# Kernel tuning notes

Hardware: AMD Instinct MI355X
Metric: run time of the kernel (lower is better)

## Reference

```python
import jax, jax.numpy as jnp
import numpy as np

NUM_QUBITS = 4
NUM_LAYERS = 3


def _ry(state, theta, wire):
    # state: (N,2,2,2,2) real amplitudes; RY(theta) on `wire` (angle scalar or (N,))
    st = jnp.moveaxis(state, wire + 1, -1)
    c = jnp.cos(theta * 0.5)
    s = jnp.sin(theta * 0.5)
    if jnp.ndim(c) == 1:  # per-sample angle -> broadcast over remaining qubit axes
        shape = (c.shape[0],) + (1,) * (st.ndim - 2)
        c = c.reshape(shape)
        s = s.reshape(shape)
    s0, s1 = st[..., 0], st[..., 1]
    new = jnp.stack([c * s0 - s * s1, s * s0 + c * s1], axis=-1)
    return jnp.moveaxis(new, -1, wire + 1)


def _cnot(state, control, target):
    st = jnp.moveaxis(state, (control + 1, target + 1), (-2, -1))
    new = jnp.stack([st[..., 0, :], st[..., 1, ::-1]], axis=-2)
    return jnp.moveaxis(new, (-2, -1), (control + 1, target + 1))


def _circuit(angles, params):
    # angles: (N,4) input rotations; params: (L,4,1) shared variational angles
    N = angles.shape[0]
    state = jnp.zeros((N, 2, 2, 2, 2), angles.dtype).at[:, 0, 0, 0, 0].set(1.0)
    for q in range(NUM_QUBITS):
        state = _ry(state, angles[:, q], q)
    for l in range(NUM_LAYERS):
        for q in range(NUM_QUBITS):
            state = _ry(state, params[l, q, 0], q)
        for q in range(NUM_QUBITS - 1):
            state = _cnot(state, q, q + 1)
    probs = state * state  # amplitudes are real (only RY/CNOT)
    meas = []
    for w in range(NUM_QUBITS):
        axes = tuple(a for a in range(1, NUM_QUBITS + 1) if a != w + 1)
        p = probs.sum(axes)  # (N,2)
        meas.append(p[:, 0] - p[:, 1])  # <Z_w>
    return jnp.stack(meas, axis=-1)  # (N,4)


def setup_inputs() -> dict:
    key = jax.random.key(0)
    k1, k2, k3, k4, k5 = jax.random.split(key, 5)
    B = 8192
    return {
        "x": jax.random.uniform(k1, (B, 1, 28, 28), dtype=jnp.float32),
        "params": jax.random.normal(k2, (NUM_LAYERS, NUM_QUBITS, 1), dtype=jnp.float32),
        "res_w": jax.random.normal(k3, (4, 1, 1, 1), dtype=jnp.float32),
        "cls_w": jax.random.normal(k4, (10, 784), dtype=jnp.float32) * 0.03,
        "cls_b": jax.random.normal(k5, (10,), dtype=jnp.float32) * 0.03,
    }


def reference(x, params, res_w, cls_w, cls_b):
    B = x.shape[0]
    img = x.reshape(B, 28, 28)
    # extract 2x2 patches, element order (r,c),(r,c+1),(r+1,c),(r+1,c+1)
    patches = img.reshape(B, 14, 2, 14, 2).transpose(0, 1, 3, 2, 4).reshape(B, 196, 4)
    # per-patch-index min/max over batch and the 4 elements (matches patch.min()/max())
    mn = patches.min(axis=(0, 2), keepdims=True)
    mx = patches.max(axis=(0, 2), keepdims=True)
    ang = (patches - mn) / (mx - mn + 1e-8) * jnp.pi
    meas = _circuit(ang.reshape(B * 196, 4), params)  # (B*196, 4)
    out = meas.reshape(B, 196 * 4).reshape(B, 4, 14, 14)  # matches torch.cat(...).view
    # res_conv: 1x1 conv, stride 2, no bias -> strided pixel scaled per out-channel
    res = img[:, ::2, ::2][:, None, :, :] * res_w.reshape(1, 4, 1, 1)
    out = out + res
    logits = out.reshape(B, -1) @ cls_w.T + cls_b
    return jax.nn.log_softmax(logits, axis=-1)
```

## Files before the change

kernel.cpp:

```cpp
#include <hip/hip_runtime.h>
#include <math.h>

#define NP 196
#define PI_F 3.14159265358979323846f

__device__ __forceinline__ unsigned fkey(float f) {
  unsigned u = __float_as_uint(f);
  return u ^ ((unsigned)((int)u >> 31) | 0x80000000u);
}
__device__ __forceinline__ float funkey(unsigned k) {
  unsigned u = (k & 0x80000000u) ? (k ^ 0x80000000u) : ~k;
  return __uint_as_float(u);
}

__global__ void __launch_bounds__(256) precompute_kernel(
    const float* __restrict__ params, const float* __restrict__ res_w,
    const float* __restrict__ cls_w, float* __restrict__ U,
    float* __restrict__ W2, unsigned* __restrict__ mn,
    unsigned* __restrict__ mx) {
  const int tid = threadIdx.x;
  if (blockIdx.x == 0) {
    if (tid < NP) { mn[tid] = 0xFFFFFFFFu; mx[tid] = 0u; }
    if (tid < 16) {
      float cp[12], sp[12];
#pragma unroll
      for (int l = 0; l < 12; ++l) __sincosf(0.5f * params[l], &sp[l], &cp[l]);
      float st[16];
#pragma unroll
      for (int i = 0; i < 16; ++i) st[i] = 0.f;
      st[tid] = 1.f;
#pragma unroll
      for (int l = 0; l < 3; ++l) {
#pragma unroll
        for (int q = 0; q < 4; ++q) {
          const float cq = cp[l * 4 + q], sq = sp[l * 4 + q];
          const int m = 8 >> q;
#pragma unroll
          for (int idx = 0; idx < 16; ++idx) {
            if (idx & m) continue;
            float v0 = st[idx], v1 = st[idx | m];
            st[idx] = cq * v0 - sq * v1;
            st[idx | m] = sq * v0 + cq * v1;
          }
        }
#pragma unroll
        for (int q = 0; q < 3; ++q) {
          const int mc = 8 >> q, mt = 4 >> q;
#pragma unroll
          for (int idx = 0; idx < 16; ++idx) {
            if ((idx & mc) && !(idx & mt)) {
              float t0 = st[idx];
              st[idx] = st[idx | mt];
              st[idx | mt] = t0;
            }
          }
        }
      }
#pragma unroll
      for (int i = 0; i < 16; ++i) U[i * 16 + tid] = st[i];
    }
  }
  for (int t = blockIdx.x * 256 + tid; t < 10 * NP; t += 8 * 256) {
    int k = t / NP, p = t - k * NP;
    float s = 0.f;
#pragma unroll
    for (int c = 0; c < 4; ++c) s += res_w[c] * cls_w[k * 784 + c * NP + p];
    W2[t] = s;
  }
}

__global__ void __launch_bounds__(256) minmax_kernel(
    const float* __restrict__ x, unsigned* __restrict__ mn,
    unsigned* __restrict__ mx, int imgs, int B) {
  __shared__ float pmn[392], pmx[392];
  const int t = threadIdx.x;
  const int img0 = blockIdx.x * imgs;
  if (t < NP) {
    const float* base = x + (size_t)img0 * 784 + 4 * t;
    float mn0 = 3.4e38f, mx0 = -3.4e38f, mn1 = 3.4e38f, mx1 = -3.4e38f;
    const int nimg = (img0 + imgs <= B) ? imgs : (B - img0);
#pragma unroll 4
    for (int m = 0; m < nimg; ++m) {
      float4 v = *(const float4*)(base + (size_t)m * 784);
      mn0 = fminf(mn0, fminf(v.x, v.y));
      mx0 = fmaxf(mx0, fmaxf(v.x, v.y));
      mn1 = fminf(mn1, fminf(v.z, v.w));
      mx1 = fmaxf(mx1, fmaxf(v.z, v.w));
    }
    const int r = (4 * t) / 28;
    const int jj = ((4 * t) - 28 * r) >> 1;
    pmn[r * 14 + jj] = mn0;
    pmx[r * 14 + jj] = mx0;
    pmn[r * 14 + jj + 1] = mn1;
    pmx[r * 14 + jj + 1] = mx1;
  }
  __syncthreads();
  if (t < NP) {
    const int i = t / 14, j = t - i * 14;
    const int f0 = (2 * i) * 14 + j, f1 = f0 + 14;
    atomicMin(&mn[t], fkey(fminf(pmn[f0], pmn[f1])));
    atomicMax(&mx[t], fkey(fmaxf(pmx[f0], pmx[f1])));
  }
}

__global__ void __launch_bounds__(256, 6) circuit_kernel(
    const float* __restrict__ x, const unsigned* __restrict__ mnk,
    const unsigned* __restrict__ mxk, const float* __restrict__ Ug,
    float4* __restrict__ gmeas, int G) {
  __shared__ float sU[256];
  __shared__ float smn[NP], ssc[NP];
  const int tid = threadIdx.x;
  sU[tid] = Ug[tid];
  if (tid < NP) {
    const float mnv = funkey(mnk[tid]);
    const float mxv = funkey(mxk[tid]);
    smn[tid] = mnv;
    ssc[tid] = (0.5f * PI_F) / (mxv - mnv + 1e-8f);
  }
  __syncthreads();

  const int g = blockIdx.x * 256 + tid;
  if (g >= G) return;
  const int b = g / NP;
  const int p = g - b * NP;
  const int i = p / 14, j = p - i * 14;

  const float* px = x + (size_t)b * 784 + (2 * i) * 28 + 2 * j;
  const float2 r0 = *(const float2*)px;
  const float2 r1 = *(const float2*)(px + 28);
  const float mnv = smn[p], sc = ssc[p];

  float cc[4], ss[4];
  __sincosf((r0.x - mnv) * sc, &ss[0], &cc[0]);
  __sincosf((r0.y - mnv) * sc, &ss[1], &cc[1]);
  __sincosf((r1.x - mnv) * sc, &ss[2], &cc[2]);
  __sincosf((r1.y - mnv) * sc, &ss[3], &cc[3]);

  float st[16];
  {
    const float A[4] = {cc[0] * cc[1], cc[0] * ss[1], ss[0] * cc[1], ss[0] * ss[1]};
    const float Bq[4] = {cc[2] * cc[3], cc[2] * ss[3], ss[2] * cc[3], ss[2] * ss[3]};
#pragma unroll
    for (int idx = 0; idx < 16; ++idx) st[idx] = A[idx >> 2] * Bq[idx & 3];
  }

  float z0 = 0.f, z1 = 0.f, z2 = 0.f, z3 = 0.f;
#pragma unroll
  for (int i2 = 0; i2 < 16; ++i2) {
    const float4 u0 = *(const float4*)&sU[i2 * 16 + 0];
    const float4 u1 = *(const float4*)&sU[i2 * 16 + 4];
    const float4 u2 = *(const float4*)&sU[i2 * 16 + 8];
    const float4 u3 = *(const float4*)&sU[i2 * 16 + 12];
    float f = u0.x * st[0];
    f = fmaf(u0.y, st[1], f);
    f = fmaf(u0.z, st[2], f);
    f = fmaf(u0.w, st[3], f);
    f = fmaf(u1.x, st[4], f);
    f = fmaf(u1.y, st[5], f);
    f = fmaf(u1.z, st[6], f);
    f = fmaf(u1.w, st[7], f);
    f = fmaf(u2.x, st[8], f);
    f = fmaf(u2.y, st[9], f);
    f = fmaf(u2.z, st[10], f);
    f = fmaf(u2.w, st[11], f);
    f = fmaf(u3.x, st[12], f);
    f = fmaf(u3.y, st[13], f);
    f = fmaf(u3.z, st[14], f);
    f = fmaf(u3.w, st[15], f);
    if (!(i2 & 8)) z0 = fmaf(f, f, z0);
    if (!(i2 & 4)) z1 = fmaf(f, f, z1);
    if (!(i2 & 2)) z2 = fmaf(f, f, z2);
    if (!(i2 & 1)) z3 = fmaf(f, f, z3);
  }
  gmeas[g] = make_float4(fmaf(2.f, z0, -1.f), fmaf(2.f, z1, -1.f),
                         fmaf(2.f, z2, -1.f), fmaf(2.f, z3, -1.f));
}

__global__ void __launch_bounds__(256) cls_kernel(
    const float4* __restrict__ gmeas, const float* __restrict__ x,
    const float* __restrict__ W2, const float4* __restrict__ cls_w4,
    const float* __restrict__ cls_b, float* __restrict__ out, int B) {
  const int wv = (blockIdx.x * 256 + threadIdx.x) >> 6;
  const int lane = threadIdx.x & 63;
  if (wv >= B) return;
  const float4* mrow = gmeas + (size_t)wv * NP;
  const float* xrow = x + (size_t)wv * 784;

  float acc[10];
#pragma unroll
  for (int k = 0; k < 10; ++k) acc[k] = 0.f;

  for (int t4 = lane; t4 < NP; t4 += 64) {
    const float4 v = mrow[t4];
#pragma unroll
    for (int k = 0; k < 10; ++k) {
      const float4 w = cls_w4[k * NP + t4];
      acc[k] = fmaf(v.x, w.x, fmaf(v.y, w.y, fmaf(v.z, w.z, fmaf(v.w, w.w, acc[k]))));
    }
  }
  for (int p = lane; p < NP; p += 64) {
    const int i = p / 14, j = p - i * 14;
    const float v = xrow[(2 * i) * 28 + 2 * j];
#pragma unroll
    for (int k = 0; k < 10; ++k) acc[k] = fmaf(v, W2[k * NP + p], acc[k]);
  }
#pragma unroll
  for (int k = 0; k < 10; ++k) {
    float a = acc[k];
#pragma unroll
    for (int off = 32; off > 0; off >>= 1) a += __shfl_down(a, off, 64);
    acc[k] = a;
  }
  if (lane == 0) {
    float lg[10];
#pragma unroll
    for (int k = 0; k < 10; ++k) lg[k] = acc[k] + cls_b[k];
    float m = lg[0];
#pragma unroll
    for (int k = 1; k < 10; ++k) m = fmaxf(m, lg[k]);
    float s = 0.f;
#pragma unroll
    for (int k = 0; k < 10; ++k) s += __expf(lg[k] - m);
    const float lse = m + __logf(s);
#pragma unroll
    for (int k = 0; k < 10; ++k) out[(size_t)wv * 10 + k] = lg[k] - lse;
  }
}

extern "C" void kernel_launch(void* const* d_in, const int* in_sizes, int n_in,
                              void* d_out, int out_size, void* d_ws, size_t ws_size,
                              hipStream_t stream) {
  const float* x      = (const float*)d_in[0];
  const float* params = (const float*)d_in[1];
  const float* res_w  = (const float*)d_in[2];
  const float* cls_w  = (const float*)d_in[3];
  const float* cls_b  = (const float*)d_in[4];
  float* out = (float*)d_out;
  const int B = in_sizes[0] / 784;

  unsigned* mn = (unsigned*)d_ws;
  unsigned* mx = mn + NP;
  float* U  = (float*)(mx + NP);
  float* W2 = U + 256;
  float* gmeas = W2 + 10 * NP;

  precompute_kernel<<<8, 256, 0, stream>>>(params, res_w, cls_w, U, W2, mn, mx);

  const int imgs = 16;
  const int nblk1 = (B + imgs - 1) / imgs;
  minmax_kernel<<<nblk1, 256, 0, stream>>>(x, mn, mx, imgs, B);

  const int G = B * NP;
  circuit_kernel<<<(G + 255) / 256, 256, 0, stream>>>(x, mn, mx, U, (float4*)gmeas, G);

  cls_kernel<<<(B * 64 + 255) / 256, 256, 0, stream>>>((const float4*)gmeas, x, W2,
                                                       (const float4*)cls_w, cls_b, out, B);
}
```

Measured before the change: 131.2 us.

## Fuse all stages into one cooperative persistent kernel with grid syncs

Replaces the four launches (precompute, minmax, circuit, classifier) with a single cooperative kernel of 512 persistent blocks that use grid.sync between phases. The min/max reduction now writes per-block partials and reduces them in a second phase instead of using global atomics. The circuit phase processes two samples per thread for more instruction-level parallelism, with split FMA chains. This removes launch gaps and atomic contention, but adds grid-wide barriers and a fixed grid size that may under-occupy the GPU.

```diff
diff --git a/kernel.cpp b/kernel.cpp
--- a/kernel.cpp
+++ b/kernel.cpp
@@ -1,8 +1,12 @@
 #include <hip/hip_runtime.h>
+#include <hip/hip_cooperative_groups.h>
 #include <math.h>
+
+namespace cg = cooperative_groups;
 
 #define NP 196
 #define PI_F 3.14159265358979323846f
+#define GRID 512
 
 __device__ __forceinline__ unsigned fkey(float f) {
   unsigned u = __float_as_uint(f);
@@ -13,73 +17,104 @@
   return __uint_as_float(u);
 }
 
-__global__ void __launch_bounds__(256) precompute_kernel(
-    const float* __restrict__ params, const float* __restrict__ res_w,
-    const float* __restrict__ cls_w, float* __restrict__ U,
-    float* __restrict__ W2, unsigned* __restrict__ mn,
-    unsigned* __restrict__ mx) {
+struct Samp {
+  float st[16];
+  const float* px;
+};
+
+__device__ __forceinline__ void load_state(const float* __restrict__ x,
+                                           const float* __restrict__ smn,
+                                           const float* __restrict__ ssc,
+                                           int g, float st[16]) {
+  const int b = g / NP;
+  const int p = g - b * NP;
+  const int i = p / 14, j = p - i * 14;
+  const float* px = x + (size_t)b * 784 + (2 * i) * 28 + 2 * j;
+  const float2 r0 = *(const float2*)px;
+  const float2 r1 = *(const float2*)(px + 28);
+  const float mnv = smn[p], sc = ssc[p];
+  float cc[4], ss[4];
+  __sincosf((r0.x - mnv) * sc, &ss[0], &cc[0]);
+  __sincosf((r0.y - mnv) * sc, &ss[1], &cc[1]);
+  __sincosf((r1.x - mnv) * sc, &ss[2], &cc[2]);
+  __sincosf((r1.y - mnv) * sc, &ss[3], &cc[3]);
+  const float A[4] = {cc[0] * cc[1], cc[0] * ss[1], ss[0] * cc[1], ss[0] * ss[1]};
+  const float Bq[4] = {cc[2] * cc[3], cc[2] * ss[3], ss[2] * cc[3], ss[2] * ss[3]};
+#pragma unroll
+  for (int idx = 0; idx < 16; ++idx) st[idx] = A[idx >> 2] * Bq[idx & 3];
+}
+
+__global__ void __launch_bounds__(256, 4) fused_kernel(
+    const float* __restrict__ x, const float* __restrict__ params,
+    const float* __restrict__ res_w, const float* __restrict__ cls_w,
+    const float* __restrict__ cls_b, float* __restrict__ out,
+    float* __restrict__ Ug, float* __restrict__ W2,
+    float* __restrict__ mnf, float* __restrict__ scf,
+    unsigned* __restrict__ pmn_g, unsigned* __restrict__ pmx_g,
+    float4* __restrict__ gmeas, int B, int ipb) {
+  cg::grid_group grid = cg::this_grid();
   const int tid = threadIdx.x;
-  if (blockIdx.x == 0) {
-    if (tid < NP) { mn[tid] = 0xFFFFFFFFu; mx[tid] = 0u; }
-    if (tid < 16) {
-      float cp[12], sp[12];
-#pragma unroll
-      for (int l = 0; l < 12; ++l) __sincosf(0.5f * params[l], &sp[l], &cp[l]);
-      float st[16];
-#pragma unroll
-      for (int i = 0; i < 16; ++i) st[i] = 0.f;
-      st[tid] = 1.f;
-#pragma unroll
-      for (int l = 0; l < 3; ++l) {
-#pragma unroll
-        for (int q = 0; q < 4; ++q) {
-          const float cq = cp[l * 4 + q], sq = sp[l * 4 + q];
-          const int m = 8 >> q;
-#pragma unroll
-          for (int idx = 0; idx < 16; ++idx) {
-            if (idx & m) continue;
-            float v0 = st[idx], v1 = st[idx | m];
-            st[idx] = cq * v0 - sq * v1;
-            st[idx | m] = sq * v0 + cq * v1;
-          }
+  const int blk = blockIdx.x;
+  const int lane = tid & 63;
+  const int wave = tid >> 6;
+
+  __shared__ float pmn[392], pmx[392];
+  __shared__ float sU[256];
+  __shared__ float smn[NP], ssc[NP];
+  __shared__ unsigned rmn[4], rmx[4];
+
+  if (blk == 0 && tid < 16) {
+    float cp[12], sp[12];
+#pragma unroll
+    for (int l = 0; l < 12; ++l) __sincosf(0.5f * params[l], &sp[l], &cp[l]);
+    float st[16];
+#pragma unroll
+    for (int i = 0; i < 16; ++i) st[i] = 0.f;
+    st[tid] = 1.f;
+#pragma unroll
+    for (int l = 0; l < 3; ++l) {
+#pragma unroll
+      for (int q = 0; q < 4; ++q) {
+        const float cq = cp[l * 4 + q], sq = sp[l * 4 + q];
+        const int m = 8 >> q;
+#pragma unroll
+        for (int idx = 0; idx < 16; ++idx) {
+          if (idx & m) continue;
+          float v0 = st[idx], v1 = st[idx | m];
+          st[idx] = cq * v0 - sq * v1;
+          st[idx | m] = sq * v0 + cq * v1;
         }
-#pragma unroll
-        for (int q = 0; q < 3; ++q) {
-          const int mc = 8 >> q, mt = 4 >> q;
-#pragma unroll
-          for (int idx = 0; idx < 16; ++idx) {
-            if ((idx & mc) && !(idx & mt)) {
-              float t0 = st[idx];
-              st[idx] = st[idx | mt];
-              st[idx | mt] = t0;
-            }
+      }
+#pragma unroll
+      for (int q = 0; q < 3; ++q) {
+        const int mc = 8 >> q, mt = 4 >> q;
+#pragma unroll
+        for (int idx = 0; idx < 16; ++idx) {
+          if ((idx & mc) && !(idx & mt)) {
+            float t0 = st[idx];
+            st[idx] = st[idx | mt];
+            st[idx | mt] = t0;
           }
         }
       }
-#pragma unroll
-      for (int i = 0; i < 16; ++i) U[i * 16 + tid] = st[i];
-    }
-  }
-  for (int t = blockIdx.x * 256 + tid; t < 10 * NP; t += 8 * 256) {
+    }
+#pragma unroll
+    for (int i = 0; i < 16; ++i) Ug[i * 16 + tid] = st[i];
+  }
+
+  for (int t = blk * 256 + tid; t < 10 * NP; t += GRID * 256) {
     int k = t / NP, p = t - k * NP;
     float s = 0.f;
 #pragma unroll
     for (int c = 0; c < 4; ++c) s += res_w[c] * cls_w[k * 784 + c * NP + p];
     W2[t] = s;
   }
-}
-
-__global__ void __launch_bounds__(256) minmax_kernel(
-    const float* __restrict__ x, unsigned* __restrict__ mn,
-    unsigned* __restrict__ mx, int imgs, int B) {
-  __shared__ float pmn[392], pmx[392];
-  const int t = threadIdx.x;
-  const int img0 = blockIdx.x * imgs;
-  if (t < NP) {
-    const float* base = x + (size_t)img0 * 784 + 4 * t;
+
+  if (tid < NP) {
+    const int img0 = blk * ipb;
+    const int nimg = min(ipb, B - img0);
+    const float* base = x + (size_t)img0 * 784 + 4 * tid;
     float mn0 = 3.4e38f, mx0 = -3.4e38f, mn1 = 3.4e38f, mx1 = -3.4e38f;
-    const int nimg = (img0 + imgs <= B) ? imgs : (B - img0);
-#pragma unroll 4
     for (int m = 0; m < nimg; ++m) {
       float4 v = *(const float4*)(base + (size_t)m * 784);
       mn0 = fminf(mn0, fminf(v.x, v.y));
@@ -87,143 +122,161 @@
       mn1 = fminf(mn1, fminf(v.z, v.w));
       mx1 = fmaxf(mx1, fmaxf(v.z, v.w));
     }
-    const int r = (4 * t) / 28;
-    const int jj = ((4 * t) - 28 * r) >> 1;
+    const int r = (4 * tid) / 28;
+    const int jj = ((4 * tid) - 28 * r) >> 1;
     pmn[r * 14 + jj] = mn0;
     pmx[r * 14 + jj] = mx0;
     pmn[r * 14 + jj + 1] = mn1;
     pmx[r * 14 + jj + 1] = mx1;
   }
   __syncthreads();
-  if (t < NP) {
-    const int i = t / 14, j = t - i * 14;
+  if (tid < NP) {
+    const int i = tid / 14, j = tid - i * 14;
     const int f0 = (2 * i) * 14 + j, f1 = f0 + 14;
-    atomicMin(&mn[t], fkey(fminf(pmn[f0], pmn[f1])));
-    atomicMax(&mx[t], fkey(fmaxf(pmx[f0], pmx[f1])));
-  }
-}
-
-__global__ void __launch_bounds__(256, 6) circuit_kernel(
-    const float* __restrict__ x, const unsigned* __restrict__ mnk,
-    const unsigned* __restrict__ mxk, const float* __restrict__ Ug,
-    float4* __restrict__ gmeas, int G) {
-  __shared__ float sU[256];
-  __shared__ float smn[NP], ssc[NP];
-  const int tid = threadIdx.x;
+    pmn_g[blk * NP + tid] = fkey(fminf(pmn[f0], pmn[f1]));
+    pmx_g[blk * NP + tid] = fkey(fmaxf(pmx[f0], pmx[f1]));
+  }
+
+  grid.sync();
+
+  if (blk < NP) {
+    unsigned kmn = 0xFFFFFFFFu, kmx = 0u;
+    for (int w = tid; w < GRID; w += 256) {
+      kmn = min(kmn, pmn_g[w * NP + blk]);
+      kmx = max(kmx, pmx_g[w * NP + blk]);
+    }
+#pragma unroll
+    for (int off = 32; off > 0; off >>= 1) {
+      kmn = min(kmn, (unsigned)__shfl_down(kmn, off, 64));
+      kmx = max(kmx, (unsigned)__shfl_down(kmx, off, 64));
+    }
+    if (lane == 0) { rmn[wave] = kmn; rmx[wave] = kmx; }
+    __syncthreads();
+    if (tid == 0) {
+      unsigned fmn = min(min(rmn[0], rmn[1]), min(rmn[2], rmn[3]));
+      unsigned fmx = max(max(rmx[0], rmx[1]), max(rmx[2], rmx[3]));
+      const float mnv = funkey(fmn), mxv = funkey(fmx);
+      mnf[blk] = mnv;
+      scf[blk] = (0.5f * PI_F) / (mxv - mnv + 1e-8f);
+    }
+  }
+
+  grid.sync();
+
   sU[tid] = Ug[tid];
-  if (tid < NP) {
-    const float mnv = funkey(mnk[tid]);
-    const float mxv = funkey(mxk[tid]);
-    smn[tid] = mnv;
-    ssc[tid] = (0.5f * PI_F) / (mxv - mnv + 1e-8f);
-  }
+  if (tid < NP) { smn[tid] = mnf[tid]; ssc[tid] = scf[tid]; }
   __syncthreads();
 
-  const int g = blockIdx.x * 256 + tid;
-  if (g >= G) return;
-  const int b = g / NP;
-  const int p = g - b * NP;
-  const int i = p / 14, j = p - i * 14;
-
-  const float* px = x + (size_t)b * 784 + (2 * i) * 28 + 2 * j;
-  const float2 r0 = *(const float2*)px;
-  const float2 r1 = *(const float2*)(px + 28);
-  const float mnv = smn[p], sc = ssc[p];
-
-  float cc[4], ss[4];
-  __sincosf((r0.x - mnv) * sc, &ss[0], &cc[0]);
-  __sincosf((r0.y - mnv) * sc, &ss[1], &cc[1]);
-  __sincosf((r1.x - mnv) * sc, &ss[2], &cc[2]);
-  __sincosf((r1.y - mnv) * sc, &ss[3], &cc[3]);
-
-  float st[16];
-  {
-    const float A[4] = {cc[0] * cc[1], cc[0] * ss[1], ss[0] * cc[1], ss[0] * ss[1]};
-    const float Bq[4] = {cc[2] * cc[3], cc[2] * ss[3], ss[2] * cc[3], ss[2] * ss[3]};
-#pragma unroll
-    for (int idx = 0; idx < 16; ++idx) st[idx] = A[idx >> 2] * Bq[idx & 3];
-  }
-
-  float z0 = 0.f, z1 = 0.f, z2 = 0.f, z3 = 0.f;
-#pragma unroll
-  for (int i2 = 0; i2 < 16; ++i2) {
-    const float4 u0 = *(const float4*)&sU[i2 * 16 + 0];
-    const float4 u1 = *(const float4*)&sU[i2 * 16 + 4];
-    const float4 u2 = *(const float4*)&sU[i2 * 16 + 8];
-    const float4 u3 = *(const float4*)&sU[i2 * 16 + 12];
-    float f = u0.x * st[0];
-    f = fmaf(u0.y, st[1], f);
-    f = fmaf(u0.z, st[2], f);
-    f = fmaf(u0.w, st[3], f);
-    f = fmaf(u1.x, st[4], f);
-    f = fmaf(u1.y, st[5], f);
-    f = fmaf(u1.z, st[6], f);
-    f = fmaf(u1.w, st[7], f);
-    f = fmaf(u2.x, st[8], f);
-    f = fmaf(u2.y, st[9], f);
-    f = fmaf(u2.z, st[10], f);
-    f = fmaf(u2.w, st[11], f);
-    f = fmaf(u3.x, st[12], f);
-    f = fmaf(u3.y, st[13], f);
-    f = fmaf(u3.z, st[14], f);
-    f = fmaf(u3.w, st[15], f);
-    if (!(i2 & 8)) z0 = fmaf(f, f, z0);
-    if (!(i2 & 4)) z1 = fmaf(f, f, z1);
-    if (!(i2 & 2)) z2 = fmaf(f, f, z2);
-    if (!(i2 & 1)) z3 = fmaf(f, f, z3);
-  }
-  gmeas[g] = make_float4(fmaf(2.f, z0, -1.f), fmaf(2.f, z1, -1.f),
-                         fmaf(2.f, z2, -1.f), fmaf(2.f, z3, -1.f));
-}
-
-__global__ void __launch_bounds__(256) cls_kernel(
-    const float4* __restrict__ gmeas, const float* __restrict__ x,
-    const float* __restrict__ W2, const float4* __restrict__ cls_w4,
-    const float* __restrict__ cls_b, float* __restrict__ out, int B) {
-  const int wv = (blockIdx.x * 256 + threadIdx.x) >> 6;
-  const int lane = threadIdx.x & 63;
-  if (wv >= B) return;
-  const float4* mrow = gmeas + (size_t)wv * NP;
-  const float* xrow = x + (size_t)wv * 784;
-
-  float acc[10];
-#pragma unroll
-  for (int k = 0; k < 10; ++k) acc[k] = 0.f;
-
-  for (int t4 = lane; t4 < NP; t4 += 64) {
-    const float4 v = mrow[t4];
+  const int G = B * NP;
+  const int nGB = (G + 255) / 256;
+  for (int gb = blk; gb < nGB; gb += 2 * GRID) {
+    const int g0 = gb * 256 + tid;
+    const int gb1 = gb + GRID;
+    const bool has1 = gb1 < nGB;
+    const int g1 = (has1 ? gb1 : gb) * 256 + tid;
+
+    float st0[16], st1[16];
+    load_state(x, smn, ssc, g0, st0);
+    load_state(x, smn, ssc, g1, st1);
+
+    float z0a = 0.f, z1a = 0.f, z2a = 0.f, z3a = 0.f;
+    float z0b = 0.f, z1b = 0.f, z2b = 0.f, z3b = 0.f;
+#pragma unroll
+    for (int i2 = 0; i2 < 16; ++i2) {
+      const float4 u0 = *(const float4*)&sU[i2 * 16 + 0];
+      const float4 u1 = *(const float4*)&sU[i2 * 16 + 4];
+      const float4 u2 = *(const float4*)&sU[i2 * 16 + 8];
+      const float4 u3 = *(const float4*)&sU[i2 * 16 + 12];
+      float fa = u0.x * st0[0];
+      fa = fmaf(u0.y, st0[1], fa);
+      fa = fmaf(u0.z, st0[2], fa);
+      fa = fmaf(u0.w, st0[3], fa);
+      float fb = u1.x * st0[4];
+      fb = fmaf(u1.y, st0[5], fb);
+      fb = fmaf(u1.z, st0[6], fb);
+      fb = fmaf(u1.w, st0[7], fb);
+      float fc = u2.x * st0[8];
+      fc = fmaf(u2.y, st0[9], fc);
+      fc = fmaf(u2.z, st0[10], fc);
+      fc = fmaf(u2.w, st0[11], fc);
+      float fd = u3.x * st0[12];
+      fd = fmaf(u3.y, st0[13], fd);
+      fd = fmaf(u3.z, st0[14], fd);
+      fd = fmaf(u3.w, st0[15], fd);
+      const float fA = (fa + fb) + (fc + fd);
+      float ga = u0.x * st1[0];
+      ga = fmaf(u0.y, st1[1], ga);
+      ga = fmaf(u0.z, st1[2], ga);
+      ga = fmaf(u0.w, st1[3], ga);
+      float gb_ = u1.x * st1[4];
+      gb_ = fmaf(u1.y, st1[5], gb_);
+      gb_ = fmaf(u1.z, st1[6], gb_);
+      gb_ = fmaf(u1.w, st1[7], gb_);
+      float gc = u2.x * st1[8];
+      gc = fmaf(u2.y, st1[9], gc);
+      gc = fmaf(u2.z, st1[10], gc);
+      gc = fmaf(u2.w, st1[11], gc);
+      float gd = u3.x * st1[12];
+      gd = fmaf(u3.y, st1[13], gd);
+      gd = fmaf(u3.z, st1[14], gd);
+      gd = fmaf(u3.w, st1[15], gd);
+      const float fB = (ga + gb_) + (gc + gd);
+      if (!(i2 & 8)) { z0a = fmaf(fA, fA, z0a); z0b = fmaf(fB, fB, z0b); }
+      if (!(i2 & 4)) { z1a = fmaf(fA, fA, z1a); z1b = fmaf(fB, fB, z1b); }
+      if (!(i2 & 2)) { z2a = fmaf(fA, fA, z2a); z2b = fmaf(fB, fB, z2b); }
+      if (!(i2 & 1)) { z3a = fmaf(fA, fA, z3a); z3b = fmaf(fB, fB, z3b); }
+    }
+    gmeas[g0] = make_float4(fmaf(2.f, z0a, -1.f), fmaf(2.f, z1a, -1.f),
+                            fmaf(2.f, z2a, -1.f), fmaf(2.f, z3a, -1.f));
+    if (has1)
+      gmeas[g1] = make_float4(fmaf(2.f, z0b, -1.f), fmaf(2.f, z1b, -1.f),
+                              fmaf(2.f, z2b, -1.f), fmaf(2.f, z3b, -1.f));
+  }
+
+  grid.sync();
+
+  const float4* cls_w4 = (const float4*)cls_w;
+  for (int img = blk * 4 + wave; img < B; img += GRID * 4) {
+    const float4* mrow = gmeas + (size_t)img * NP;
+    const float* xrow = x + (size_t)img * 784;
+    float acc[10];
+#pragma unroll
+    for (int k = 0; k < 10; ++k) acc[k] = 0.f;
+    for (int t4 = lane; t4 < NP; t4 += 64) {
+      const float4 v = mrow[t4];
+#pragma unroll
+      for (int k = 0; k < 10; ++k) {
+        const float4 w = cls_w4[k * NP + t4];
+        acc[k] = fmaf(v.x, w.x, fmaf(v.y, w.y, fmaf(v.z, w.z, fmaf(v.w, w.w, acc[k]))));
+      }
+    }
+    for (int p = lane; p < NP; p += 64) {
+      const int i = p / 14, j = p - i * 14;
+      const float v = xrow[(2 * i) * 28 + 2 * j];
+#pragma unroll
+      for (int k = 0; k < 10; ++k) acc[k] = fmaf(v, W2[k * NP + p], acc[k]);
+    }
 #pragma unroll
     for (int k = 0; k < 10; ++k) {
-      const float4 w = cls_w4[k * NP + t4];
-      acc[k] = fmaf(v.x, w.x, fmaf(v.y, w.y, fmaf(v.z, w.z, fmaf(v.w, w.w, acc[k]))));
-    }
-  }
-  for (int p = lane; p < NP; p += 64) {
-    const int i = p / 14, j = p - i * 14;
-    const float v = xrow[(2 * i) * 28 + 2 * j];
-#pragma unroll
-    for (int k = 0; k < 10; ++k) acc[k] = fmaf(v, W2[k * NP + p], acc[k]);
-  }
-#pragma unroll
-  for (int k = 0; k < 10; ++k) {
-    float a = acc[k];
-#pragma unroll
-    for (int off = 32; off > 0; off >>= 1) a += __shfl_down(a, off, 64);
-    acc[k] = a;
-  }
-  if (lane == 0) {
-    float lg[10];
-#pragma unroll
-    for (int k = 0; k < 10; ++k) lg[k] = acc[k] + cls_b[k];
-    float m = lg[0];
-#pragma unroll
-    for (int k = 1; k < 10; ++k) m = fmaxf(m, lg[k]);
-    float s = 0.f;
-#pragma unroll
-    for (int k = 0; k < 10; ++k) s += __expf(lg[k] - m);
-    const float lse = m + __logf(s);
-#pragma unroll
-    for (int k = 0; k < 10; ++k) out[(size_t)wv * 10 + k] = lg[k] - lse;
+      float a = acc[k];
+#pragma unroll
+      for (int off = 32; off > 0; off >>= 1) a += __shfl_down(a, off, 64);
+      acc[k] = a;
+    }
+    if (lane == 0) {
+      float lg[10];
+#pragma unroll
+      for (int k = 0; k < 10; ++k) lg[k] = acc[k] + cls_b[k];
+      float m = lg[0];
+#pragma unroll
+      for (int k = 1; k < 10; ++k) m = fmaxf(m, lg[k]);
+      float s = 0.f;
+#pragma unroll
+      for (int k = 0; k < 10; ++k) s += __expf(lg[k] - m);
+      const float lse = m + __logf(s);
+#pragma unroll
+      for (int k = 0; k < 10; ++k) out[(size_t)img * 10 + k] = lg[k] - lse;
+    }
   }
 }
 
@@ -236,23 +289,22 @@
   const float* cls_w  = (const float*)d_in[3];
   const float* cls_b  = (const float*)d_in[4];
   float* out = (float*)d_out;
-  const int B = in_sizes[0] / 784;
-
-  unsigned* mn = (unsigned*)d_ws;
-  unsigned* mx = mn + NP;
-  float* U  = (float*)(mx + NP);
-  float* W2 = U + 256;
-  float* gmeas = W2 + 10 * NP;
-
-  precompute_kernel<<<8, 256, 0, stream>>>(params, res_w, cls_w, U, W2, mn, mx);
-
-  const int imgs = 16;
-  const int nblk1 = (B + imgs - 1) / imgs;
-  minmax_kernel<<<nblk1, 256, 0, stream>>>(x, mn, mx, imgs, B);
-
-  const int G = B * NP;
-  circuit_kernel<<<(G + 255) / 256, 256, 0, stream>>>(x, mn, mx, U, (float4*)gmeas, G);
-
-  cls_kernel<<<(B * 64 + 255) / 256, 256, 0, stream>>>((const float4*)gmeas, x, W2,
-                                                       (const float4*)cls_w, cls_b, out, B);
-}
+  int B = in_sizes[0] / 784;
+
+  float4* gmeas = (float4*)d_ws;
+  float* Ug  = (float*)d_ws + (size_t)B * 784;
+  float* W2  = Ug + 256;
+  float* mnf = W2 + 10 * NP;
+  float* scf = mnf + NP;
+  unsigned* pmn_g = (unsigned*)(scf + NP);
+  unsigned* pmx_g = pmn_g + GRID * NP;
+
+  int ipb = (B + GRID - 1) / GRID;
+
+  void* args[] = {(void*)&x, (void*)&params, (void*)&res_w, (void*)&cls_w,
+                  (void*)&cls_b, (void*)&out, (void*)&Ug, (void*)&W2,
+                  (void*)&mnf, (void*)&scf, (void*)&pmn_g, (void*)&pmx_g,
+                  (void*)&gmeas, (void*)&B, (void*)&ipb};
+  hipLaunchCooperativeKernel((const void*)fused_kernel, dim3(GRID), dim3(256),
+                             args, 0, stream);
+}
```

After: 474.1 us. +261.3%, slower.
